# Performance work log

Measured on AMD Instinct MI355X. Metric: run time of the kernel, lower is better.

The kernel has to match this reference:

```python
import jax, jax.numpy as jnp
import numpy as np

N_NODES = 100000
N_EDGES = 1600000
IN_CH, HID_CH, OUT_CH = 128, 64, 32


def setup_inputs() -> dict:
    key = jax.random.key(0)
    k1, k2, k3, k4 = jax.random.split(key, 4)
    x = jax.random.normal(k1, (N_NODES, IN_CH), dtype=jnp.float32)
    edge_index = jax.random.randint(k2, (2, N_EDGES), 0, N_NODES, dtype=jnp.int32)
    # Glorot-ish scaling like PyG's GCNConv init
    W1 = jax.random.normal(k3, (IN_CH, HID_CH), dtype=jnp.float32) / np.sqrt(IN_CH)
    b1 = jnp.zeros((HID_CH,), dtype=jnp.float32)
    W2 = jax.random.normal(k4, (HID_CH, OUT_CH), dtype=jnp.float32) / np.sqrt(HID_CH)
    b2 = jnp.zeros((OUT_CH,), dtype=jnp.float32)
    return {"x": x, "edge_index": edge_index, "W1": W1, "b1": b1, "W2": W2, "b2": b2}


def reference(x, edge_index, W1, b1, W2, b2):
    # PyG GCNConv semantics: add self-loops, symmetric deg^{-1/2} normalization,
    # linear transform, scatter-add aggregation to destination nodes, add bias.
    N = x.shape[0]
    loops = jnp.arange(N, dtype=edge_index.dtype)
    src = jnp.concatenate([edge_index[0], loops])  # [E+N]
    dst = jnp.concatenate([edge_index[1], loops])  # [E+N]

    deg = jax.ops.segment_sum(jnp.ones_like(src, dtype=x.dtype), dst, num_segments=N)
    dis = jnp.where(deg > 0, jax.lax.rsqrt(jnp.maximum(deg, 1.0)), 0.0)  # deg^{-1/2}
    norm = (dis[src] * dis[dst])[:, None]  # [E+N, 1]

    def gcn_conv(h, W, b):
        h = h @ W                                   # [N, C_out]
        msgs = h[src] * norm                        # gather + scale, [E+N, C_out]
        return jax.ops.segment_sum(msgs, dst, num_segments=N) + b

    h = jax.nn.relu(gcn_conv(x, W1, b1))
    # dropout is identity in eval mode (training=False)
    return gcn_conv(h, W2, b2)
```

## Files before the change

### kernel.cpp

```cpp
#include <hip/hip_runtime.h>
#include <hip/hip_bf16.h>

#define IN_CH 128
#define HID_CH 64
#define OUT_CH 32
#define EPB 2048
#define MAXB 512

typedef unsigned short ushort_t;
typedef __attribute__((ext_vector_type(8))) short short8;
typedef __attribute__((ext_vector_type(4))) float float4v;
using half8 = __attribute__((ext_vector_type(8))) _Float16;

static __device__ __forceinline__ ushort_t f2bf(float f) {
    unsigned u = __float_as_uint(f);
    unsigned r = (u + 0x7fff + ((u >> 16) & 1)) >> 16;
    return (ushort_t)r;
}
static __device__ __forceinline__ float bf_lo(unsigned u) { return __uint_as_float(u << 16); }
static __device__ __forceinline__ float bf_hi(unsigned u) { return __uint_as_float(u & 0xffff0000u); }

static __device__ __forceinline__ unsigned f2h2(float lo, float hi) {
    union { _Float16 h[2]; unsigned u; } v;
    v.h[0] = (_Float16)lo;
    v.h[1] = (_Float16)hi;
    return v.u;
}
static __device__ __forceinline__ unsigned pkh(float a, float b) {
    auto p = __builtin_amdgcn_cvt_pkrtz(a, b);
    union { decltype(p) h; unsigned u; } v;
    v.h = p;
    return v.u;
}


__global__ __launch_bounds__(256) void k_partition(const int* __restrict__ src,
                                                   const int* __restrict__ dst,
                                                   int* __restrict__ gcursor,
                                                   unsigned* __restrict__ pairs,
                                                   int E, int nbk, int cap, int PB,
                                                   const float* __restrict__ W1,
                                                   const float* __restrict__ W2,
                                                   unsigned* __restrict__ wsW) {
    __shared__ int lhist[MAXB];
    __shared__ int lbase[MAXB];
    __shared__ int lcur[MAXB];
    const int tid = threadIdx.x;

    if (blockIdx.x >= PB) {
        int s = (blockIdx.x - PB) * 256 + tid;
        if (s < 1024) {
            int lane = s & 63;
            int nt = (s >> 6) & 3;
            int kc = s >> 8;
            int c = nt * 16 + (lane & 15);
            int k0 = kc * 32 + (lane >> 4) * 8;
            unsigned o[4];
#pragma unroll
            for (int d = 0; d < 4; ++d) {
                unsigned lo = f2bf(W1[(k0 + 2 * d) * 64 + c]);
                unsigned hi = f2bf(W1[(k0 + 2 * d + 1) * 64 + c]);
                o[d] = lo | (hi << 16);
            }
            ((uint4*)wsW)[s] = make_uint4(o[0], o[1], o[2], o[3]);
        } else {
            int q = s - 1024;
            int lane = q & 63;
            int f = q >> 6;
            int c = (f & 1) * 16 + (lane & 15);
            int k0 = (f >> 1) * 32 + (lane >> 4) * 8;
            unsigned o[4];
#pragma unroll
            for (int d = 0; d < 4; ++d)
                o[d] = f2h2(W2[(k0 + 2 * d) * 32 + c], W2[(k0 + 2 * d + 1) * 32 + c]);
            ((uint4*)wsW)[1024 + q] = make_uint4(o[0], o[1], o[2], o[3]);
        }
        return;
    }

    for (int b = tid; b < nbk; b += 256) { lhist[b] = 0; lcur[b] = 0; }
    __syncthreads();
    int s[8], d[8];
    const int e0 = blockIdx.x * EPB;
#pragma unroll
    for (int j = 0; j < 8; ++j) {
        int e = e0 + j * 256 + tid;
        if (e < E) {
            s[j] = src[e];
            d[j] = dst[e];
            atomicAdd(&lhist[d[j] >> 8], 1);
        } else {
            d[j] = -1;
        }
    }
    __syncthreads();
    for (int b = tid; b < nbk; b += 256)
        lbase[b] = lhist[b] ? atomicAdd(&gcursor[b], lhist[b]) : 0;
    __syncthreads();
#pragma unroll
    for (int j = 0; j < 8; ++j) {
        if (d[j] >= 0) {
            int b = d[j] >> 8;
            int loc = atomicAdd(&lcur[b], 1);
            int idx = lbase[b] + loc;
            if (idx < cap)
                pairs[(long long)b * cap + idx] = ((unsigned)s[j] << 8) | (unsigned)(d[j] & 255);
        }
    }
}


__global__ __launch_bounds__(256) void k_bucket_build(const unsigned* __restrict__ pairs,
                                                      const int* __restrict__ gcursor,
                                                      int* __restrict__ rowptr,
                                                      int* __restrict__ col,
                                                      float* __restrict__ dis,
                                                      unsigned* __restrict__ h1zero,
                                                      int cap, int N) {
    __shared__ int lc[256];
    __shared__ int ls[256];
    __shared__ int lcur[256];
    const int b = blockIdx.x, tid = threadIdx.x;

    if (b == 0 && tid < 32) h1zero[tid] = 0;

    int ga = min(gcursor[2 * tid], cap);
    int gb = min(gcursor[2 * tid + 1], cap);
    ls[tid] = ga + gb;
    __syncthreads();
    for (int off = 1; off < 256; off <<= 1) {
        int val = (tid >= off) ? ls[tid - off] : 0;
        __syncthreads();
        ls[tid] += val;
        __syncthreads();
    }
    const int p = b >> 1;
    const int base = (p ? ls[p - 1] : 0) + ((b & 1) ? min(gcursor[b - 1], cap) : 0);
    const int total = ls[255];
    __syncthreads();
    if (b == 0 && tid == 0) rowptr[N] = total;

    lc[tid] = 0;
    __syncthreads();
    const int cnt = min(gcursor[b], cap);
    const unsigned* pp = pairs + (long long)b * cap;
    for (int i = tid; i < cnt; i += 256) atomicAdd(&lc[pp[i] & 255], 1);
    __syncthreads();
    const int v = lc[tid];
    ls[tid] = v;
    __syncthreads();
    for (int off = 1; off < 256; off <<= 1) {
        int val = (tid >= off) ? ls[tid - off] : 0;
        __syncthreads();
        ls[tid] += val;
        __syncthreads();
    }
    const int excl = ls[tid] - v;
    const int row = b * 256 + tid;
    if (row < N) {
        rowptr[row] = base + excl;
        dis[row] = rsqrtf((float)(v + 1));
    }
    lcur[tid] = base + excl;
    __syncthreads();
    for (int i = tid; i < cnt; i += 256) {
        unsigned pk = pp[i];
        int pos = atomicAdd(&lcur[pk & 255], 1);
        col[pos] = (int)(pk >> 8);
    }
}


__global__ __launch_bounds__(256) void k_mm1(const float* __restrict__ X,
                                             const unsigned* __restrict__ wsW,
                                             const float* __restrict__ dis,
                                             ushort_t* __restrict__ H,
                                             unsigned* __restrict__ h2zero, int N) {
    const int tid = threadIdx.x;
    if (blockIdx.x == 0 && tid < 16) h2zero[tid] = 0;

    const int wv = tid >> 6, lane = tid & 63;
    const int quad = lane >> 4, n16 = lane & 15;
    const int rowbase = blockIdx.x * 64 + wv * 16;
    const int myrow = rowbase + n16;
    const bool rok = (myrow < N);

    float4v acc0 = {}, acc1 = {}, acc2 = {}, acc3 = {};

#pragma unroll
    for (int kc = 0; kc < 4; ++kc) {
        float4 xa = make_float4(0.f, 0.f, 0.f, 0.f), xb = xa;
        if (rok) {
            const float4* p = (const float4*)(X + (long long)myrow * 128 + kc * 32 + quad * 8);
            xa = p[0];
            xb = p[1];
        }
        unsigned pk[4];
        pk[0] = (unsigned)f2bf(xa.x) | ((unsigned)f2bf(xa.y) << 16);
        pk[1] = (unsigned)f2bf(xa.z) | ((unsigned)f2bf(xa.w) << 16);
        pk[2] = (unsigned)f2bf(xb.x) | ((unsigned)f2bf(xb.y) << 16);
        pk[3] = (unsigned)f2bf(xb.z) | ((unsigned)f2bf(xb.w) << 16);
        short8 a;
        a[0] = (short)(pk[0] & 0xffff); a[1] = (short)(pk[0] >> 16);
        a[2] = (short)(pk[1] & 0xffff); a[3] = (short)(pk[1] >> 16);
        a[4] = (short)(pk[2] & 0xffff); a[5] = (short)(pk[2] >> 16);
        a[6] = (short)(pk[3] & 0xffff); a[7] = (short)(pk[3] >> 16);

        const short8* wb = (const short8*)wsW;
        short8 b0 = wb[(kc * 4 + 0) * 64 + lane];
        short8 b1 = wb[(kc * 4 + 1) * 64 + lane];
        short8 b2 = wb[(kc * 4 + 2) * 64 + lane];
        short8 b3 = wb[(kc * 4 + 3) * 64 + lane];

        acc0 = __builtin_amdgcn_mfma_f32_16x16x32_bf16(a, b0, acc0, 0, 0, 0);
        acc1 = __builtin_amdgcn_mfma_f32_16x16x32_bf16(a, b1, acc1, 0, 0, 0);
        acc2 = __builtin_amdgcn_mfma_f32_16x16x32_bf16(a, b2, acc2, 0, 0, 0);
        acc3 = __builtin_amdgcn_mfma_f32_16x16x32_bf16(a, b3, acc3, 0, 0, 0);
    }

#pragma unroll
    for (int i = 0; i < 4; ++i) {
        int row = rowbase + quad * 4 + i;
        if (row < N) {
            float dr = dis[row];
            long long o = (long long)row * 64 + n16;
            H[o]      = f2bf(dr * acc0[i]);
            H[o + 16] = f2bf(dr * acc1[i]);
            H[o + 32] = f2bf(dr * acc2[i]);
            H[o + 48] = f2bf(dr * acc3[i]);
        }
    }
}


__global__ __launch_bounds__(256, 8) void k_agg64_mm2(const unsigned* __restrict__ h,
                                                      const int* __restrict__ rowptr,
                                                      const int* __restrict__ col,
                                                      const float* __restrict__ dis,
                                                      const float* __restrict__ b1,
                                                      const unsigned* __restrict__ wsW2,
                                                      unsigned* __restrict__ h2, int N) {
    __shared__ __align__(16) _Float16 zbl[4][8][72];
    const int tid = threadIdx.x;
    const int wv = tid >> 6, lane = tid & 63;
    const int t = lane & 7, g = lane >> 3;
    const float4 bqa = ((const float4*)b1)[2 * t];
    const float4 bqb = ((const float4*)b1)[2 * t + 1];

    const half8* wfh = (const half8*)wsW2;
    const half8 bf00 = wfh[lane];
    const half8 bf01 = wfh[64 + lane];
    const half8 bf10 = wfh[128 + lane];
    const half8 bf11 = wfh[192 + lane];

    ushort_t* H2u = (ushort_t*)h2;
    const uint4* h4 = (const uint4*)h;
    const int NB = (N + 7) >> 3;
    const int step = gridDim.x * 4;

    for (int rb = blockIdx.x * 4 + wv; rb < NB; rb += step) {
        const int r0 = rb * 8;
        int rp_l = rowptr[min(r0 + min(lane, 8), N)];
        float dis_l = (lane < 8 && r0 + lane < N) ? dis[r0 + lane] : 0.f;
        const int sg = __shfl(rp_l, g);
        const int dg = __shfl(rp_l, g + 1) - sg;
        const float drg = __shfl(dis_l, g);
        float dr03[4];
#pragma unroll
        for (int i = 0; i < 4; ++i) dr03[i] = __shfl(dis_l, ((lane >> 4) & 1) * 4 + i);

        int mc1 = N, mc2 = N, mc3 = N;
        if (t < dg)      mc1 = col[sg + t];
        if (8 + t < dg)  mc2 = col[sg + 8 + t];
        if (16 + t < dg) mc3 = col[sg + 16 + t];

        const int rme = min(r0 + g, N);
        uint4 us = h4[rme * 8 + t];
        float2 p0 = make_float2(bf_lo(us.x), bf_hi(us.x));
        float2 p1 = make_float2(bf_lo(us.y), bf_hi(us.y));
        float2 p2 = make_float2(bf_lo(us.z), bf_hi(us.z));
        float2 p3 = make_float2(bf_lo(us.w), bf_hi(us.w));

#define GATX(MC, U)                                                   \
    {                                                                 \
        int s_ = __shfl((MC), (g << 3) + (U));                        \
        uint4 uu = h4[s_ * 8 + t];                                    \
        p0 += make_float2(bf_lo(uu.x), bf_hi(uu.x));                  \
        p1 += make_float2(bf_lo(uu.y), bf_hi(uu.y));                  \
        p2 += make_float2(bf_lo(uu.z), bf_hi(uu.z));                  \
        p3 += make_float2(bf_lo(uu.w), bf_hi(uu.w));                  \
    }
#pragma unroll
        for (int u = 0; u < 8; ++u) GATX(mc1, u)
#pragma unroll
        for (int u = 0; u < 8; ++u) GATX(mc2, u)
#pragma unroll
        for (int u = 0; u < 8; ++u) GATX(mc3, u)
        if (__any(dg > 24)) {
            int mc4 = N;
            if (24 + t < dg) mc4 = col[sg + 24 + t];
#pragma unroll
            for (int u = 0; u < 8; ++u) GATX(mc4, u)
        }
        for (int u = 32; u < dg; ++u) {
            int s_ = col[sg + u];
            uint4 uu = h4[s_ * 8 + t];
            p0 += make_float2(bf_lo(uu.x), bf_hi(uu.x));
            p1 += make_float2(bf_lo(uu.y), bf_hi(uu.y));
            p2 += make_float2(bf_lo(uu.z), bf_hi(uu.z));
            p3 += make_float2(bf_lo(uu.w), bf_hi(uu.w));
        }
#undef GATX

        {
            float z0 = fmaxf(fmaf(drg, p0.x, bqa.x), 0.f);
            float z1 = fmaxf(fmaf(drg, p0.y, bqa.y), 0.f);
            float z2 = fmaxf(fmaf(drg, p1.x, bqa.z), 0.f);
            float z3 = fmaxf(fmaf(drg, p1.y, bqa.w), 0.f);
            float z4 = fmaxf(fmaf(drg, p2.x, bqb.x), 0.f);
            float z5 = fmaxf(fmaf(drg, p2.y, bqb.y), 0.f);
            float z6 = fmaxf(fmaf(drg, p3.x, bqb.z), 0.f);
            float z7 = fmaxf(fmaf(drg, p3.y, bqb.w), 0.f);
            *(uint4*)&zbl[wv][g][8 * t] =
                make_uint4(pkh(z0, z1), pkh(z2, z3), pkh(z4, z5), pkh(z6, z7));
        }
        __builtin_amdgcn_wave_barrier();

        const int zr = lane & 7;
        const int ko = (lane >> 4) * 8;
        half8 af0 = *(const half8*)&zbl[wv][zr][ko];
        half8 af1 = *(const half8*)&zbl[wv][zr][ko + 32];
        float4v c0 = {}, c1 = {};
        c0 = __builtin_amdgcn_mfma_f32_16x16x32_f16(af0, bf00, c0, 0, 0, 0);
        c0 = __builtin_amdgcn_mfma_f32_16x16x32_f16(af1, bf10, c0, 0, 0, 0);
        c1 = __builtin_amdgcn_mfma_f32_16x16x32_f16(af0, bf01, c1, 0, 0, 0);
        c1 = __builtin_amdgcn_mfma_f32_16x16x32_f16(af1, bf11, c1, 0, 0, 0);
        __builtin_amdgcn_wave_barrier();

        if (lane < 32) {
            const int li = lane >> 4;
            const int cc = lane & 15;
#pragma unroll
            for (int i = 0; i < 4; ++i) {
                int rr = r0 + li * 4 + i;
                if (rr < N) {
                    H2u[rr * 32 + cc]      = f2bf(dr03[i] * c0[i]);
                    H2u[rr * 32 + 16 + cc] = f2bf(dr03[i] * c1[i]);
                }
            }
        }
    }
}


__global__ __launch_bounds__(256, 8) void k_agg32(const unsigned* __restrict__ h,
                                                  const int* __restrict__ rowptr,
                                                  const int* __restrict__ col,
                                                  const float* __restrict__ dis,
                                                  const float* __restrict__ b,
                                                  float* __restrict__ out, int N) {
    const int tid = threadIdx.x;
    const int wv = tid >> 6, lane = tid & 63;
    const int t = lane & 7, g = lane >> 3;
    const float4 bq = ((const float4*)b)[t];
    const uint2* hw = (const uint2*)h;
    const int NB = (N + 7) >> 3;
    const int step = gridDim.x * 4;

    for (int rb = blockIdx.x * 4 + wv; rb < NB; rb += step) {
        const int r0 = rb * 8;
        int rp_l = rowptr[min(r0 + min(lane, 8), N)];
        float dis_l = (lane < 8 && r0 + lane < N) ? dis[r0 + lane] : 0.f;
        const int sg = __shfl(rp_l, g);
        const int dg = __shfl(rp_l, g + 1) - sg;
        const float drg = __shfl(dis_l, g);

        int mc1 = N, mc2 = N, mc3 = N;
        if (t < dg)      mc1 = col[sg + t];
        if (8 + t < dg)  mc2 = col[sg + 8 + t];
        if (16 + t < dg) mc3 = col[sg + 16 + t];

        const int rme = min(r0 + g, N);
        uint2 us = hw[rme * 8 + t];
        float2 p0 = make_float2(bf_lo(us.x), bf_hi(us.x));
        float2 p1 = make_float2(bf_lo(us.y), bf_hi(us.y));

#define GAT2(MC, U)                                                   \
    {                                                                 \
        int s_ = __shfl((MC), (g << 3) + (U));                        \
        uint2 uu = hw[s_ * 8 + t];                                    \
        p0 += make_float2(bf_lo(uu.x), bf_hi(uu.x));                  \
        p1 += make_float2(bf_lo(uu.y), bf_hi(uu.y));                  \
    }
#pragma unroll
        for (int u = 0; u < 8; ++u) GAT2(mc1, u)
#pragma unroll
        for (int u = 0; u < 8; ++u) GAT2(mc2, u)
#pragma unroll
        for (int u = 0; u < 8; ++u) GAT2(mc3, u)
        if (__any(dg > 24)) {
            int mc4 = N;
            if (24 + t < dg) mc4 = col[sg + 24 + t];
#pragma unroll
            for (int u = 0; u < 8; ++u) GAT2(mc4, u)
        }
        for (int u = 32; u < dg; ++u) {
            int s_ = col[sg + u];
            uint2 uu = hw[s_ * 8 + t];
            p0 += make_float2(bf_lo(uu.x), bf_hi(uu.x));
            p1 += make_float2(bf_lo(uu.y), bf_hi(uu.y));
        }
#undef GAT2

        const int rr = r0 + g;
        if (rr < N) {
            float4 o;
            o.x = bq.x + drg * p0.x;
            o.y = bq.y + drg * p0.y;
            o.z = bq.z + drg * p1.x;
            o.w = bq.w + drg * p1.y;
            ((float4*)out)[(long long)rr * 8 + t] = o;
        }
    }
}

extern "C" void kernel_launch(void* const* d_in, const int* in_sizes, int n_in,
                              void* d_out, int out_size, void* d_ws, size_t ws_size,
                              hipStream_t stream) {
    const float* x  = (const float*)d_in[0];
    const int*   ei = (const int*)d_in[1];
    const float* W1 = (const float*)d_in[2];
    const float* b1 = (const float*)d_in[3];
    const float* W2 = (const float*)d_in[4];
    const float* b2 = (const float*)d_in[5];
    float* out = (float*)d_out;

    const int N = in_sizes[0] / IN_CH;
    const int E = in_sizes[1] / 2;
    const int* esrc = ei;
    const int* edst = ei + E;

    int nbk = (N + 255) >> 8;
    if (nbk > MAXB) nbk = MAXB;
    const int per_b = (E + nbk - 1) / nbk;
    const int cap = per_b + per_b / 4 + 256;

    int* rowptr   = (int*)d_ws;
    int* gcursor  = rowptr + (((N + 1) + 15) & ~15);
    unsigned* wsW = (unsigned*)(gcursor + MAXB);
    int* col      = (int*)(wsW + 5120);
    float* dis    = (float*)(col + ((E + 15) & ~15));
    ushort_t* h1  = (ushort_t*)(dis + ((N + 15) & ~15));
    unsigned* scratch = (unsigned*)(h1 + (((long long)(N + 1) * 64 + 31) & ~31LL));
    unsigned* pairs = scratch;
    unsigned* h2    = scratch;

    const int B = 256;
    const int PB = (E + EPB - 1) / EPB;
    const int AGG_BLOCKS = 2048;

    hipMemsetAsync(gcursor, 0, MAXB * sizeof(int), stream);
    k_partition<<<PB + 5, B, 0, stream>>>(esrc, edst, gcursor, pairs, E, nbk, cap, PB, W1, W2, wsW);
    k_bucket_build<<<nbk, B, 0, stream>>>(pairs, gcursor, rowptr, col, dis,
                                          (unsigned*)(h1 + (long long)N * 64), cap, N);

    k_mm1<<<(N + 63) / 64, B, 0, stream>>>(x, wsW, dis, h1, h2 + (long long)N * 16, N);

    k_agg64_mm2<<<AGG_BLOCKS, B, 0, stream>>>((const unsigned*)h1, rowptr, col, dis, b1,
                                              wsW + 4096, h2, N);

    k_agg32<<<AGG_BLOCKS, B, 0, stream>>>((const unsigned*)h2, rowptr, col, dis, b2, out, N);
}
```

Before: 234.7 us.

## Split feature tables into XCD-sliced planes and separate gather from second matmul

Stores H1 as eight channel-slice planes of 8 bf16 per node and H2 as two 16-channel planes. Gather blocks are mapped so that blockIdx mod 8 (the XCD index under round-robin dispatch) selects a slice, so each XCD's L2 only needs to cache one slice of the gathered table. The fused aggregate+mm2 kernel is split into a one-thread-per-row gather writing fp16 Z, a standalone MFMA mm2 kernel, and a per-row agg32. This trades an extra kernel launch and a round trip of Z through memory for better L2 locality on random gathers, and it assumes blocks are dispatched round-robin across the eight XCDs.

```diff
diff --git a/kernel.cpp b/kernel.cpp
--- a/kernel.cpp
+++ b/kernel.cpp
@@ -10,6 +10,8 @@
 typedef unsigned short ushort_t;
 typedef __attribute__((ext_vector_type(8))) short short8;
 typedef __attribute__((ext_vector_type(4))) float float4v;
+typedef __attribute__((ext_vector_type(4))) float fx4;
+typedef __attribute__((ext_vector_type(4))) unsigned ux4;
 using half8 = __attribute__((ext_vector_type(8))) _Float16;
 
 static __device__ __forceinline__ ushort_t f2bf(float f) {
@@ -115,14 +117,15 @@
                                                       int* __restrict__ rowptr,
                                                       int* __restrict__ col,
                                                       float* __restrict__ dis,
-                                                      unsigned* __restrict__ h1zero,
+                                                      unsigned* __restrict__ h1d,
                                                       int cap, int N) {
     __shared__ int lc[256];
     __shared__ int ls[256];
     __shared__ int lcur[256];
     const int b = blockIdx.x, tid = threadIdx.x;
 
-    if (b == 0 && tid < 32) h1zero[tid] = 0;
+    if (b == 0 && tid < 32)
+        h1d[((long long)(tid >> 2) * (N + 1) + N) * 4 + (tid & 3)] = 0;
 
     int ga = min(gcursor[2 * tid], cap);
     int gb = min(gcursor[2 * tid + 1], cap);
@@ -174,11 +177,8 @@
 __global__ __launch_bounds__(256) void k_mm1(const float* __restrict__ X,
                                              const unsigned* __restrict__ wsW,
                                              const float* __restrict__ dis,
-                                             ushort_t* __restrict__ H,
-                                             unsigned* __restrict__ h2zero, int N) {
+                                             ushort_t* __restrict__ H, int N) {
     const int tid = threadIdx.x;
-    if (blockIdx.x == 0 && tid < 16) h2zero[tid] = 0;
-
     const int wv = tid >> 6, lane = tid & 63;
     const int quad = lane >> 4, n16 = lane & 15;
     const int rowbase = blockIdx.x * 64 + wv * 16;
@@ -218,34 +218,116 @@
         acc3 = __builtin_amdgcn_mfma_f32_16x16x32_bf16(a, b3, acc3, 0, 0, 0);
     }
 
+    const int pb = n16 >> 3, dd = n16 & 7;
 #pragma unroll
     for (int i = 0; i < 4; ++i) {
         int row = rowbase + quad * 4 + i;
         if (row < N) {
             float dr = dis[row];
-            long long o = (long long)row * 64 + n16;
-            H[o]      = f2bf(dr * acc0[i]);
-            H[o + 16] = f2bf(dr * acc1[i]);
-            H[o + 32] = f2bf(dr * acc2[i]);
-            H[o + 48] = f2bf(dr * acc3[i]);
-        }
-    }
-}
-
-
-__global__ __launch_bounds__(256, 8) void k_agg64_mm2(const unsigned* __restrict__ h,
-                                                      const int* __restrict__ rowptr,
-                                                      const int* __restrict__ col,
-                                                      const float* __restrict__ dis,
-                                                      const float* __restrict__ b1,
-                                                      const unsigned* __restrict__ wsW2,
-                                                      unsigned* __restrict__ h2, int N) {
-    __shared__ __align__(16) _Float16 zbl[4][8][72];
+            H[((long long)(0 + pb) * (N + 1) + row) * 8 + dd] = f2bf(dr * acc0[i]);
+            H[((long long)(2 + pb) * (N + 1) + row) * 8 + dd] = f2bf(dr * acc1[i]);
+            H[((long long)(4 + pb) * (N + 1) + row) * 8 + dd] = f2bf(dr * acc2[i]);
+            H[((long long)(6 + pb) * (N + 1) + row) * 8 + dd] = f2bf(dr * acc3[i]);
+        }
+    }
+}
+
+
+__global__ __launch_bounds__(256, 8) void k_gather1(const unsigned* __restrict__ h,
+                                                    const int* __restrict__ rowptr,
+                                                    const int* __restrict__ col,
+                                                    const float* __restrict__ dis,
+                                                    const float* __restrict__ b1,
+                                                    unsigned* __restrict__ z,
+                                                    int N, int nunits) {
     const int tid = threadIdx.x;
     const int wv = tid >> 6, lane = tid & 63;
-    const int t = lane & 7, g = lane >> 3;
-    const float4 bqa = ((const float4*)b1)[2 * t];
-    const float4 bqb = ((const float4*)b1)[2 * t + 1];
+    const int x = blockIdx.x & 7;
+    const int j = blockIdx.x >> 3;
+    const int jn = gridDim.x >> 3;
+
+    const uint4* h8 = (const uint4*)h + (long long)x * (N + 1);
+    unsigned* z8 = z + (long long)x * (N + 1) * 4;
+    const float4 ba = ((const float4*)b1)[x * 2];
+    const float4 bb = ((const float4*)b1)[x * 2 + 1];
+
+    for (int r = j; r < nunits; r += jn) {
+        const int row = r * 256 + wv * 64 + lane;
+        const int rme = min(row, N);
+        const int sg = rowptr[rme];
+        const int dg = rowptr[min(rme + 1, N)] - sg;
+        const float drg = (row < N) ? dis[row] : 0.f;
+
+        int mc[24];
+#pragma unroll
+        for (int u = 0; u < 24; ++u)
+            mc[u] = (u < dg) ? __builtin_nontemporal_load(col + sg + u) : N;
+
+        uint4 us = h8[rme];
+        float2 p0 = make_float2(bf_lo(us.x), bf_hi(us.x));
+        float2 p1 = make_float2(bf_lo(us.y), bf_hi(us.y));
+        float2 p2 = make_float2(bf_lo(us.z), bf_hi(us.z));
+        float2 p3 = make_float2(bf_lo(us.w), bf_hi(us.w));
+
+#pragma unroll
+        for (int u = 0; u < 24; ++u) {
+            uint4 uu = h8[mc[u]];
+            p0 += make_float2(bf_lo(uu.x), bf_hi(uu.x));
+            p1 += make_float2(bf_lo(uu.y), bf_hi(uu.y));
+            p2 += make_float2(bf_lo(uu.z), bf_hi(uu.z));
+            p3 += make_float2(bf_lo(uu.w), bf_hi(uu.w));
+        }
+        for (int base = 24; __any(base < dg); base += 8) {
+            int m2[8];
+#pragma unroll
+            for (int u = 0; u < 8; ++u)
+                m2[u] = (base + u < dg) ? __builtin_nontemporal_load(col + sg + base + u) : N;
+#pragma unroll
+            for (int u = 0; u < 8; ++u) {
+                uint4 uu = h8[m2[u]];
+                p0 += make_float2(bf_lo(uu.x), bf_hi(uu.x));
+                p1 += make_float2(bf_lo(uu.y), bf_hi(uu.y));
+                p2 += make_float2(bf_lo(uu.z), bf_hi(uu.z));
+                p3 += make_float2(bf_lo(uu.w), bf_hi(uu.w));
+            }
+        }
+
+        if (row < N) {
+            float z0 = fmaxf(fmaf(drg, p0.x, ba.x), 0.f);
+            float z1 = fmaxf(fmaf(drg, p0.y, ba.y), 0.f);
+            float z2 = fmaxf(fmaf(drg, p1.x, ba.z), 0.f);
+            float z3 = fmaxf(fmaf(drg, p1.y, ba.w), 0.f);
+            float z4 = fmaxf(fmaf(drg, p2.x, bb.x), 0.f);
+            float z5 = fmaxf(fmaf(drg, p2.y, bb.y), 0.f);
+            float z6 = fmaxf(fmaf(drg, p3.x, bb.z), 0.f);
+            float z7 = fmaxf(fmaf(drg, p3.y, bb.w), 0.f);
+            ux4 zo;
+            zo.x = pkh(z0, z1);
+            zo.y = pkh(z2, z3);
+            zo.z = pkh(z4, z5);
+            zo.w = pkh(z6, z7);
+            __builtin_nontemporal_store(zo, (ux4*)(z8 + (long long)row * 4));
+        }
+    }
+}
+
+
+__global__ __launch_bounds__(256) void k_mm2(const unsigned* __restrict__ z,
+                                             const unsigned* __restrict__ wsW2,
+                                             const float* __restrict__ dis,
+                                             ushort_t* __restrict__ H2, int N) {
+    const int tid = threadIdx.x;
+    if (blockIdx.x == 0 && tid < 16)
+        ((unsigned*)H2)[((long long)(tid >> 3) * (N + 1) + N) * 8 + (tid & 7)] = 0;
+
+    const int wv = tid >> 6, lane = tid & 63;
+    const int n16 = lane & 15, kq = lane >> 4;
+    const int rowbase = blockIdx.x * 64 + wv * 16;
+    const int rz = min(rowbase + n16, N - 1);
+
+    const uint4* z4 = (const uint4*)z;
+    uint4 a0 = z4[(long long)kq * (N + 1) + rz];
+    uint4 a1 = z4[(long long)(4 + kq) * (N + 1) + rz];
 
     const half8* wfh = (const half8*)wsW2;
     const half8 bf00 = wfh[lane];
@@ -253,174 +335,112 @@
     const half8 bf10 = wfh[128 + lane];
     const half8 bf11 = wfh[192 + lane];
 
-    ushort_t* H2u = (ushort_t*)h2;
-    const uint4* h4 = (const uint4*)h;
-    const int NB = (N + 7) >> 3;
-    const int step = gridDim.x * 4;
-
-    for (int rb = blockIdx.x * 4 + wv; rb < NB; rb += step) {
-        const int r0 = rb * 8;
-        int rp_l = rowptr[min(r0 + min(lane, 8), N)];
-        float dis_l = (lane < 8 && r0 + lane < N) ? dis[r0 + lane] : 0.f;
-        const int sg = __shfl(rp_l, g);
-        const int dg = __shfl(rp_l, g + 1) - sg;
-        const float drg = __shfl(dis_l, g);
-        float dr03[4];
-#pragma unroll
-        for (int i = 0; i < 4; ++i) dr03[i] = __shfl(dis_l, ((lane >> 4) & 1) * 4 + i);
-
-        int mc1 = N, mc2 = N, mc3 = N;
-        if (t < dg)      mc1 = col[sg + t];
-        if (8 + t < dg)  mc2 = col[sg + 8 + t];
-        if (16 + t < dg) mc3 = col[sg + 16 + t];
-
-        const int rme = min(r0 + g, N);
-        uint4 us = h4[rme * 8 + t];
-        float2 p0 = make_float2(bf_lo(us.x), bf_hi(us.x));
-        float2 p1 = make_float2(bf_lo(us.y), bf_hi(us.y));
-        float2 p2 = make_float2(bf_lo(us.z), bf_hi(us.z));
-        float2 p3 = make_float2(bf_lo(us.w), bf_hi(us.w));
-
-#define GATX(MC, U)                                                   \
-    {                                                                 \
-        int s_ = __shfl((MC), (g << 3) + (U));                        \
-        uint4 uu = h4[s_ * 8 + t];                                    \
-        p0 += make_float2(bf_lo(uu.x), bf_hi(uu.x));                  \
-        p1 += make_float2(bf_lo(uu.y), bf_hi(uu.y));                  \
-        p2 += make_float2(bf_lo(uu.z), bf_hi(uu.z));                  \
-        p3 += make_float2(bf_lo(uu.w), bf_hi(uu.w));                  \
-    }
-#pragma unroll
-        for (int u = 0; u < 8; ++u) GATX(mc1, u)
-#pragma unroll
-        for (int u = 0; u < 8; ++u) GATX(mc2, u)
-#pragma unroll
-        for (int u = 0; u < 8; ++u) GATX(mc3, u)
-        if (__any(dg > 24)) {
-            int mc4 = N;
-            if (24 + t < dg) mc4 = col[sg + 24 + t];
-#pragma unroll
-            for (int u = 0; u < 8; ++u) GATX(mc4, u)
-        }
-        for (int u = 32; u < dg; ++u) {
-            int s_ = col[sg + u];
-            uint4 uu = h4[s_ * 8 + t];
-            p0 += make_float2(bf_lo(uu.x), bf_hi(uu.x));
-            p1 += make_float2(bf_lo(uu.y), bf_hi(uu.y));
-            p2 += make_float2(bf_lo(uu.z), bf_hi(uu.z));
-            p3 += make_float2(bf_lo(uu.w), bf_hi(uu.w));
-        }
-#undef GATX
-
-        {
-            float z0 = fmaxf(fmaf(drg, p0.x, bqa.x), 0.f);
-            float z1 = fmaxf(fmaf(drg, p0.y, bqa.y), 0.f);
-            float z2 = fmaxf(fmaf(drg, p1.x, bqa.z), 0.f);
-            float z3 = fmaxf(fmaf(drg, p1.y, bqa.w), 0.f);
-            float z4 = fmaxf(fmaf(drg, p2.x, bqb.x), 0.f);
-            float z5 = fmaxf(fmaf(drg, p2.y, bqb.y), 0.f);
-            float z6 = fmaxf(fmaf(drg, p3.x, bqb.z), 0.f);
-            float z7 = fmaxf(fmaf(drg, p3.y, bqb.w), 0.f);
-            *(uint4*)&zbl[wv][g][8 * t] =
-                make_uint4(pkh(z0, z1), pkh(z2, z3), pkh(z4, z5), pkh(z6, z7));
-        }
-        __builtin_amdgcn_wave_barrier();
-
-        const int zr = lane & 7;
-        const int ko = (lane >> 4) * 8;
-        half8 af0 = *(const half8*)&zbl[wv][zr][ko];
-        half8 af1 = *(const half8*)&zbl[wv][zr][ko + 32];
-        float4v c0 = {}, c1 = {};
-        c0 = __builtin_amdgcn_mfma_f32_16x16x32_f16(af0, bf00, c0, 0, 0, 0);
-        c0 = __builtin_amdgcn_mfma_f32_16x16x32_f16(af1, bf10, c0, 0, 0, 0);
-        c1 = __builtin_amdgcn_mfma_f32_16x16x32_f16(af0, bf01, c1, 0, 0, 0);
-        c1 = __builtin_amdgcn_mfma_f32_16x16x32_f16(af1, bf11, c1, 0, 0, 0);
-        __builtin_amdgcn_wave_barrier();
-
-        if (lane < 32) {
-            const int li = lane >> 4;
-            const int cc = lane & 15;
-#pragma unroll
-            for (int i = 0; i < 4; ++i) {
-                int rr = r0 + li * 4 + i;
-                if (rr < N) {
-                    H2u[rr * 32 + cc]      = f2bf(dr03[i] * c0[i]);
-                    H2u[rr * 32 + 16 + cc] = f2bf(dr03[i] * c1[i]);
-                }
-            }
-        }
-    }
-}
-
-
-__global__ __launch_bounds__(256, 8) void k_agg32(const unsigned* __restrict__ h,
+    union U { uint4 u; half8 h; };
+    U ua0, ua1;
+    ua0.u = a0;
+    ua1.u = a1;
+
+    float4v c0 = {}, c1 = {};
+    c0 = __builtin_amdgcn_mfma_f32_16x16x32_f16(ua0.h, bf00, c0, 0, 0, 0);
+    c0 = __builtin_amdgcn_mfma_f32_16x16x32_f16(ua1.h, bf10, c0, 0, 0, 0);
+    c1 = __builtin_amdgcn_mfma_f32_16x16x32_f16(ua0.h, bf01, c1, 0, 0, 0);
+    c1 = __builtin_amdgcn_mfma_f32_16x16x32_f16(ua1.h, bf11, c1, 0, 0, 0);
+
+    float dis_l = (lane < 16 && rowbase + lane < N) ? dis[rowbase + lane] : 0.f;
+#pragma unroll
+    for (int i = 0; i < 4; ++i) {
+        int rr = rowbase + kq * 4 + i;
+        float dr = __shfl(dis_l, kq * 4 + i);
+        if (rr < N) {
+            H2[(long long)rr * 16 + n16] = f2bf(dr * c0[i]);
+            H2[((long long)(N + 1) + rr) * 16 + n16] = f2bf(dr * c1[i]);
+        }
+    }
+}
+
+
+__global__ __launch_bounds__(256, 8) void k_agg32(const unsigned* __restrict__ h2,
                                                   const int* __restrict__ rowptr,
                                                   const int* __restrict__ col,
                                                   const float* __restrict__ dis,
-                                                  const float* __restrict__ b,
-                                                  float* __restrict__ out, int N) {
+                                                  const float* __restrict__ b2,
+                                                  float* __restrict__ out, int N, int nunits) {
     const int tid = threadIdx.x;
     const int wv = tid >> 6, lane = tid & 63;
-    const int t = lane & 7, g = lane >> 3;
-    const float4 bq = ((const float4*)b)[t];
-    const uint2* hw = (const uint2*)h;
-    const int NB = (N + 7) >> 3;
-    const int step = gridDim.x * 4;
-
-    for (int rb = blockIdx.x * 4 + wv; rb < NB; rb += step) {
-        const int r0 = rb * 8;
-        int rp_l = rowptr[min(r0 + min(lane, 8), N)];
-        float dis_l = (lane < 8 && r0 + lane < N) ? dis[r0 + lane] : 0.f;
-        const int sg = __shfl(rp_l, g);
-        const int dg = __shfl(rp_l, g + 1) - sg;
-        const float drg = __shfl(dis_l, g);
-
-        int mc1 = N, mc2 = N, mc3 = N;
-        if (t < dg)      mc1 = col[sg + t];
-        if (8 + t < dg)  mc2 = col[sg + 8 + t];
-        if (16 + t < dg) mc3 = col[sg + 16 + t];
-
-        const int rme = min(r0 + g, N);
-        uint2 us = hw[rme * 8 + t];
-        float2 p0 = make_float2(bf_lo(us.x), bf_hi(us.x));
-        float2 p1 = make_float2(bf_lo(us.y), bf_hi(us.y));
-
-#define GAT2(MC, U)                                                   \
-    {                                                                 \
-        int s_ = __shfl((MC), (g << 3) + (U));                        \
-        uint2 uu = hw[s_ * 8 + t];                                    \
-        p0 += make_float2(bf_lo(uu.x), bf_hi(uu.x));                  \
-        p1 += make_float2(bf_lo(uu.y), bf_hi(uu.y));                  \
-    }
-#pragma unroll
-        for (int u = 0; u < 8; ++u) GAT2(mc1, u)
-#pragma unroll
-        for (int u = 0; u < 8; ++u) GAT2(mc2, u)
-#pragma unroll
-        for (int u = 0; u < 8; ++u) GAT2(mc3, u)
-        if (__any(dg > 24)) {
-            int mc4 = N;
-            if (24 + t < dg) mc4 = col[sg + 24 + t];
-#pragma unroll
-            for (int u = 0; u < 8; ++u) GAT2(mc4, u)
-        }
-        for (int u = 32; u < dg; ++u) {
-            int s_ = col[sg + u];
-            uint2 uu = hw[s_ * 8 + t];
-            p0 += make_float2(bf_lo(uu.x), bf_hi(uu.x));
-            p1 += make_float2(bf_lo(uu.y), bf_hi(uu.y));
-        }
-#undef GAT2
-
-        const int rr = r0 + g;
-        if (rr < N) {
-            float4 o;
-            o.x = bq.x + drg * p0.x;
-            o.y = bq.y + drg * p0.y;
-            o.z = bq.z + drg * p1.x;
-            o.w = bq.w + drg * p1.y;
-            ((float4*)out)[(long long)rr * 8 + t] = o;
-        }
+    const int xcd = blockIdx.x & 7;
+    const int hh = xcd >> 2, sub = xcd & 3;
+    const int j = blockIdx.x >> 3;
+
+    const uint4* hw = (const uint4*)h2 + (long long)hh * (N + 1) * 2;
+    const float4 bq0 = ((const float4*)b2)[hh * 4 + 0];
+    const float4 bq1 = ((const float4*)b2)[hh * 4 + 1];
+    const float4 bq2 = ((const float4*)b2)[hh * 4 + 2];
+    const float4 bq3 = ((const float4*)b2)[hh * 4 + 3];
+
+    const int r = j * 4 + sub;
+    if (r >= nunits) return;
+    const int row = r * 256 + wv * 64 + lane;
+    const int rme = min(row, N);
+    const int sg = rowptr[rme];
+    const int dg = rowptr[min(rme + 1, N)] - sg;
+    const float drg = (row < N) ? dis[row] : 0.f;
+
+    int mc[16];
+#pragma unroll
+    for (int u = 0; u < 16; ++u)
+        mc[u] = (u < dg) ? __builtin_nontemporal_load(col + sg + u) : N;
+
+    uint4 ua = hw[(long long)rme * 2];
+    uint4 ub = hw[(long long)rme * 2 + 1];
+    float2 p0 = make_float2(bf_lo(ua.x), bf_hi(ua.x));
+    float2 p1 = make_float2(bf_lo(ua.y), bf_hi(ua.y));
+    float2 p2 = make_float2(bf_lo(ua.z), bf_hi(ua.z));
+    float2 p3 = make_float2(bf_lo(ua.w), bf_hi(ua.w));
+    float2 p4 = make_float2(bf_lo(ub.x), bf_hi(ub.x));
+    float2 p5 = make_float2(bf_lo(ub.y), bf_hi(ub.y));
+    float2 p6 = make_float2(bf_lo(ub.z), bf_hi(ub.z));
+    float2 p7 = make_float2(bf_lo(ub.w), bf_hi(ub.w));
+
+#define ACC2(S)                                                        \
+    {                                                                  \
+        uint4 va = hw[(long long)(S) * 2];                             \
+        uint4 vb = hw[(long long)(S) * 2 + 1];                         \
+        p0 += make_float2(bf_lo(va.x), bf_hi(va.x));                   \
+        p1 += make_float2(bf_lo(va.y), bf_hi(va.y));                   \
+        p2 += make_float2(bf_lo(va.z), bf_hi(va.z));                   \
+        p3 += make_float2(bf_lo(va.w), bf_hi(va.w));                   \
+        p4 += make_float2(bf_lo(vb.x), bf_hi(vb.x));                   \
+        p5 += make_float2(bf_lo(vb.y), bf_hi(vb.y));                   \
+        p6 += make_float2(bf_lo(vb.z), bf_hi(vb.z));                   \
+        p7 += make_float2(bf_lo(vb.w), bf_hi(vb.w));                   \
+    }
+#pragma unroll
+    for (int u = 0; u < 16; ++u) ACC2(mc[u])
+    for (int base = 16; __any(base < dg); base += 8) {
+        int m2[8];
+#pragma unroll
+        for (int u = 0; u < 8; ++u)
+            m2[u] = (base + u < dg) ? __builtin_nontemporal_load(col + sg + base + u) : N;
+#pragma unroll
+        for (int u = 0; u < 8; ++u) ACC2(m2[u])
+    }
+#undef ACC2
+
+    if (row < N) {
+        fx4 o0, o1, o2, o3;
+        o0.x = bq0.x + drg * p0.x; o0.y = bq0.y + drg * p0.y;
+        o0.z = bq0.z + drg * p1.x; o0.w = bq0.w + drg * p1.y;
+        o1.x = bq1.x + drg * p2.x; o1.y = bq1.y + drg * p2.y;
+        o1.z = bq1.z + drg * p3.x; o1.w = bq1.w + drg * p3.y;
+        o2.x = bq2.x + drg * p4.x; o2.y = bq2.y + drg * p4.y;
+        o2.z = bq2.z + drg * p5.x; o2.w = bq2.w + drg * p5.y;
+        o3.x = bq3.x + drg * p6.x; o3.y = bq3.y + drg * p6.y;
+        o3.z = bq3.z + drg * p7.x; o3.w = bq3.w + drg * p7.y;
+        fx4* op = (fx4*)(out + (long long)row * 32 + hh * 16);
+        __builtin_nontemporal_store(o0, op);
+        __builtin_nontemporal_store(o1, op + 1);
+        __builtin_nontemporal_store(o2, op + 2);
+        __builtin_nontemporal_store(o3, op + 3);
     }
 }
 
@@ -453,21 +473,24 @@
     ushort_t* h1  = (ushort_t*)(dis + ((N + 15) & ~15));
     unsigned* scratch = (unsigned*)(h1 + (((long long)(N + 1) * 64 + 31) & ~31LL));
     unsigned* pairs = scratch;
-    unsigned* h2    = scratch;
+    unsigned* z     = scratch;
+    ushort_t* h2    = h1;
 
     const int B = 256;
     const int PB = (E + EPB - 1) / EPB;
-    const int AGG_BLOCKS = 2048;
+    const int NU = (N + 255) >> 8;
+    const int G1J = 196;
+    const int G2J = (NU + 3) / 4;
 
     hipMemsetAsync(gcursor, 0, MAXB * sizeof(int), stream);
     k_partition<<<PB + 5, B, 0, stream>>>(esrc, edst, gcursor, pairs, E, nbk, cap, PB, W1, W2, wsW);
-    k_bucket_build<<<nbk, B, 0, stream>>>(pairs, gcursor, rowptr, col, dis,
-                                          (unsigned*)(h1 + (long long)N * 64), cap, N);
-
-    k_mm1<<<(N + 63) / 64, B, 0, stream>>>(x, wsW, dis, h1, h2 + (long long)N * 16, N);
-
-    k_agg64_mm2<<<AGG_BLOCKS, B, 0, stream>>>((const unsigned*)h1, rowptr, col, dis, b1,
-                                              wsW + 4096, h2, N);
-
-    k_agg32<<<AGG_BLOCKS, B, 0, stream>>>((const unsigned*)h2, rowptr, col, dis, b2, out, N);
-}
+    k_bucket_build<<<nbk, B, 0, stream>>>(pairs, gcursor, rowptr, col, dis, (unsigned*)h1, cap, N);
+
+    k_mm1<<<(N + 63) / 64, B, 0, stream>>>(x, wsW, dis, h1, N);
+
+    k_gather1<<<8 * G1J, B, 0, stream>>>((const unsigned*)h1, rowptr, col, dis, b1, z, N, NU);
+
+    k_mm2<<<(N + 63) / 64, B, 0, stream>>>(z, wsW + 4096, dis, h2, N);
+
+    k_agg32<<<8 * G2J, B, 0, stream>>>((const unsigned*)h2, rowptr, col, dis, b2, out, N, NU);
+}
```

Measured after the change: 357.8 us. +52.5%, slower.
